# Kernel tuning notes

Measured on AMD Instinct MI355X. Metric: run time of the kernel, lower is better.

Reference implementation:

```python
import jax, jax.numpy as jnp
import numpy as np

NUM_HEAD = 16
FEAT_DIM = 1024
HEAD_DIM = FEAT_DIM // NUM_HEAD  # 64
MAX_SEQ_LEN = 2048
BATCH = 2


def setup_inputs() -> dict:
    key = jax.random.key(0)
    ks = jax.random.split(key, 6)
    x = jax.random.normal(ks[0], (BATCH, MAX_SEQ_LEN, FEAT_DIM), dtype=jnp.float32)
    # xavier_uniform: limit = sqrt(6/(fan_in+fan_out)); torch Linear weight is [out, in]
    def xavier(k, out_f, in_f):
        lim = float(np.sqrt(6.0 / (in_f + out_f)))
        return jax.random.uniform(k, (out_f, in_f), dtype=jnp.float32, minval=-lim, maxval=lim)
    W1 = xavier(ks[1], HEAD_DIM, HEAD_DIM)          # attn_mlp[0].weight
    b1 = jnp.zeros((HEAD_DIM,), dtype=jnp.float32)
    W2 = xavier(ks[2], MAX_SEQ_LEN, HEAD_DIM)       # attn_mlp[2].weight
    b2 = jnp.zeros((MAX_SEQ_LEN,), dtype=jnp.float32)
    Wv = xavier(ks[3], FEAT_DIM, FEAT_DIM)          # value_linear.weight (no bias)
    Wo = xavier(ks[4], FEAT_DIM, FEAT_DIM)          # output_linear.weight (no bias)
    return {"x": x, "W1": W1, "b1": b1, "W2": W2, "b2": b2, "Wv": Wv, "Wo": Wo}


def _split_head(t):
    b, n, _ = t.shape
    return t.reshape(b, n, NUM_HEAD, HEAD_DIM).transpose(0, 2, 1, 3)  # [b,h,n,d]


def reference(x, W1, b1, W2, b2, Wv, Wo):
    # value projection (dropout is identity in eval / p=0)
    value = x @ Wv.T                                   # [b,n,F]
    vh = _split_head(value)                            # [b,h,n,d]
    xh = _split_head(x)                                # [b,h,n,d]
    # per-head MLP -> dense attention logits [b,h,n,max_seq_len]
    hid = jax.nn.relu(jnp.einsum('bhnd,ed->bhne', xh, W1) + b1)
    logits = jnp.einsum('bhne,me->bhnm', hid, W2) + b2
    attn = jax.nn.softmax(logits, axis=-1)             # [b,h,n,m]
    out_h = jnp.einsum('bhnm,bhmd->bhnd', attn, vh)    # m == seq_len
    b_, h_, n_, d_ = out_h.shape
    out = out_h.transpose(0, 2, 1, 3).reshape(b_, n_, FEAT_DIM)
    return out @ Wo.T
```

## Files before the change

### kernel.cpp

```cpp
#include <hip/hip_runtime.h>
#include <hip/hip_bf16.h>
#include <math.h>
#include <stdint.h>


typedef __attribute__((ext_vector_type(8))) short bf16x8;
typedef __attribute__((ext_vector_type(4))) float f32x4;
typedef __attribute__((ext_vector_type(16))) float f32x16;

#define LOG2E 1.4426950408889634f

__device__ __forceinline__ unsigned short f2bf(float f) {
  union { float f; unsigned u; } v; v.f = f;
  unsigned r = v.u + 0x7FFFu + ((v.u >> 16) & 1u);
  return (unsigned short)(r >> 16);
}

__global__ __launch_bounds__(256) void conv_bf16(const float* __restrict__ src,
                                                 unsigned short* __restrict__ dst, int nq) {
  int stride = gridDim.x * blockDim.x;
  for (int q = blockIdx.x * blockDim.x + threadIdx.x; q < nq; q += stride) {
    float4 v = *(const float4*)(src + (size_t)q * 4);
    uint2 u;
    u.x = (unsigned)f2bf(v.x) | ((unsigned)f2bf(v.y) << 16);
    u.y = (unsigned)f2bf(v.z) | ((unsigned)f2bf(v.w) << 16);
    *(uint2*)(dst + (size_t)q * 4) = u;
  }
}

__global__ __launch_bounds__(256) void prep_kernel(const float* __restrict__ Wv,
                                                   const float* __restrict__ Wo,
                                                   const float* __restrict__ W2,
                                                   const float* __restrict__ W1,
                                                   const float* __restrict__ b2,
                                                   unsigned short* __restrict__ wvb,
                                                   unsigned short* __restrict__ wob,
                                                   unsigned short* __restrict__ w2b,
                                                   unsigned short* __restrict__ w1b,
                                                   float* __restrict__ eb2f,
                                                   unsigned short* __restrict__ ebb) {
  int bid = blockIdx.x;
  if (bid == 1024) {
    int i = threadIdx.x;
#pragma unroll
    for (int t = 0; t < 8; ++t) {
      int k = i * 8 + t;
      float e = __expf(b2[k]);
      eb2f[k] = e;
      ebb[k] = f2bf(e);
    }
    return;
  }
  int stride = 1024 * 256;
  for (int q = bid * 256 + threadIdx.x; q < 558080; q += stride) {
    const float* s; unsigned short* d; int o;
    if (q < 262144)      { s = Wv; d = wvb; o = q; }
    else if (q < 524288) { s = Wo; d = wob; o = q - 262144; }
    else if (q < 557056) { s = W2; d = w2b; o = q - 524288; }
    else                 { s = W1; d = w1b; o = q - 557056; }
    float4 v = *(const float4*)(s + (size_t)o * 4);
    uint2 u;
    u.x = (unsigned)f2bf(v.x) | ((unsigned)f2bf(v.y) << 16);
    u.y = (unsigned)f2bf(v.z) | ((unsigned)f2bf(v.w) << 16);
    *(uint2*)(d + (size_t)o * 4) = u;
  }
}

__device__ __forceinline__ void stage64(const char* g, size_t ldbytes, char* lds,
                                        int w, int lane) {
#pragma unroll
  for (int t = 0; t < 2; ++t) {
    int row  = w * 16 + t * 8 + (lane >> 3);
    int csrc = (lane & 7) ^ (lane >> 3);
    const char* src = g + (size_t)row * ldbytes + (csrc << 4);
    char* dst = lds + ((w * 2 + t) << 10);
    __builtin_amdgcn_global_load_lds((const __attribute__((address_space(1))) void*)src,
                                     (__attribute__((address_space(3))) void*)dst,
                                     16, 0, 0);
  }
}

__device__ __forceinline__ bf16x8 rdfrag32(const char* lds, int row, int chunk) {
  int c = chunk ^ (row & 7);
  return *(const bf16x8*)(lds + row * 128 + (c << 4));
}

__device__ __forceinline__ f32x16 loadb16(const float* p) {
  f32x16 r;
#pragma unroll
  for (int qd = 0; qd < 4; ++qd) {
    float4 v = *(const float4*)(p + qd * 8);
    r[qd * 4 + 0] = v.x; r[qd * 4 + 1] = v.y; r[qd * 4 + 2] = v.z; r[qd * 4 + 3] = v.w;
  }
  return r;
}

__device__ __forceinline__ bf16x8 pk_swap(float r0, float r1, float r2, float r3,
                                          float r4, float r5, float r6, float r7) {
  unsigned a, b, c, d;
  asm("v_cvt_pk_bf16_f32 %0, %1, %2" : "=v"(a) : "v"(r0), "v"(r1));
  asm("v_cvt_pk_bf16_f32 %0, %1, %2" : "=v"(b) : "v"(r4), "v"(r5));
  asm("v_cvt_pk_bf16_f32 %0, %1, %2" : "=v"(c) : "v"(r2), "v"(r3));
  asm("v_cvt_pk_bf16_f32 %0, %1, %2" : "=v"(d) : "v"(r6), "v"(r7));
  asm("v_permlane32_swap_b32 %0, %1" : "+v"(a), "+v"(b));
  asm("v_permlane32_swap_b32 %0, %1" : "+v"(c), "+v"(d));
  union { unsigned u[4]; bf16x8 v; } r;
  r.u[0] = a; r.u[1] = c; r.u[2] = b; r.u[3] = d;
  return r.v;
}

template<int MODE>
__global__ __launch_bounds__(256) void gemm128(const unsigned short* __restrict__ A,
                                               const unsigned short* __restrict__ B,
                                               void* __restrict__ C,
                                               const float* __restrict__ eb2f, int K) {
  __shared__ __attribute__((aligned(16))) char As[2][16384];
  __shared__ __attribute__((aligned(16))) char Bs[2][16384];
  int tid = threadIdx.x, w = tid >> 6, lane = tid & 63;
  int l31 = lane & 31, hi = lane >> 5;
  int wr = w >> 1, wc = w & 1;
  int bm = blockIdx.x, bn = blockIdx.y;
  const char* Ab = (const char*)A + (size_t)bm * 128 * (K * 2);
  const char* Bb = (const char*)B + (size_t)bn * 128 * (K * 2);
  size_t ld = (size_t)K * 2;

  f32x16 acc00 = {}, acc01 = {}, acc10 = {}, acc11 = {};
  stage64(Ab, ld, As[0], w, lane);
  stage64(Ab + 64 * ld, ld, As[0] + 8192, w, lane);
  stage64(Bb, ld, Bs[0], w, lane);
  stage64(Bb + 64 * ld, ld, Bs[0] + 8192, w, lane);
  __syncthreads();

  int nst = K >> 6;
  for (int kk = 0; kk < nst; ++kk) {
    int cur = kk & 1;
    if (kk + 1 < nst) {
      const char* An = Ab + (size_t)(kk + 1) * 128;
      const char* Bn = Bb + (size_t)(kk + 1) * 128;
      stage64(An, ld, As[cur ^ 1], w, lane);
      stage64(An + 64 * ld, ld, As[cur ^ 1] + 8192, w, lane);
      stage64(Bn, ld, Bs[cur ^ 1], w, lane);
      stage64(Bn + 64 * ld, ld, Bs[cur ^ 1] + 8192, w, lane);
    }
    __builtin_amdgcn_s_setprio(1);
#pragma unroll
    for (int ks = 0; ks < 4; ++ks) {
      bf16x8 a0 = rdfrag32(As[cur], wr * 64 + l31, ks * 2 + hi);
      bf16x8 a1 = rdfrag32(As[cur], wr * 64 + 32 + l31, ks * 2 + hi);
      bf16x8 b0 = rdfrag32(Bs[cur], wc * 64 + l31, ks * 2 + hi);
      bf16x8 b1 = rdfrag32(Bs[cur], wc * 64 + 32 + l31, ks * 2 + hi);
      acc00 = __builtin_amdgcn_mfma_f32_32x32x16_bf16(a0, b0, acc00, 0, 0, 0);
      acc01 = __builtin_amdgcn_mfma_f32_32x32x16_bf16(a0, b1, acc01, 0, 0, 0);
      acc10 = __builtin_amdgcn_mfma_f32_32x32x16_bf16(a1, b0, acc10, 0, 0, 0);
      acc11 = __builtin_amdgcn_mfma_f32_32x32x16_bf16(a1, b1, acc11, 0, 0, 0);
    }
    __builtin_amdgcn_s_setprio(0);
    __syncthreads();
  }

  if (MODE == 0) {
    unsigned short* vt = (unsigned short*)C;
#pragma unroll
    for (int i = 0; i < 2; ++i) {
      int rowb = bm * 128 + wr * 64 + i * 32;
#pragma unroll
      for (int qd = 0; qd < 4; ++qd) {
        int m0 = rowb + qd * 8 + hi * 4;
        float4 e4 = *(const float4*)(eb2f + (m0 & 2047));
        int bb = m0 >> 11, n = m0 & 2047;
#pragma unroll
        for (int j = 0; j < 2; ++j) {
          int h = bn * 2 + wc, d = j * 32 + l31;
          f32x16 a = (i == 0) ? (j == 0 ? acc00 : acc01) : (j == 0 ? acc10 : acc11);
          int r0 = qd * 4;
          uint2 u;
          u.x = (unsigned)f2bf(a[r0] * e4.x) | ((unsigned)f2bf(a[r0 + 1] * e4.y) << 16);
          u.y = (unsigned)f2bf(a[r0 + 2] * e4.z) | ((unsigned)f2bf(a[r0 + 3] * e4.w) << 16);
          *(uint2*)(vt + ((size_t)((bb * 16 + h) * 64 + d)) * 2048 + n) = u;
        }
      }
    }
  } else {
    float* Cf = (float*)C;
    int rb = bm * 128 + wr * 64, cb = bn * 128 + wc * 64;
#pragma unroll
    for (int r = 0; r < 16; ++r) {
      int row = (r & 3) + 8 * (r >> 2) + 4 * hi;
      Cf[(size_t)(rb + row) * 1024 + cb + l31]          = acc00[r];
      Cf[(size_t)(rb + row) * 1024 + cb + 32 + l31]     = acc01[r];
      Cf[(size_t)(rb + 32 + row) * 1024 + cb + l31]     = acc10[r];
      Cf[(size_t)(rb + 32 + row) * 1024 + cb + 32 + l31] = acc11[r];
    }
  }
}

__global__ __launch_bounds__(256) void flash_kernel(const unsigned short* __restrict__ xb,
                                                    const unsigned short* __restrict__ w1b,
                                                    const float* __restrict__ b1,
                                                    const unsigned short* __restrict__ w2b,
                                                    const unsigned short* __restrict__ ebb,
                                                    const unsigned short* __restrict__ vt,
                                                    unsigned short* __restrict__ aout) {
  __shared__ __attribute__((aligned(16))) char Kbuf[16384];
  __shared__ __attribute__((aligned(16))) char Vbuf[16384];
  int tid = threadIdx.x, w = tid >> 6, lane = tid & 63;
  int l31 = lane & 31, hi = lane >> 5;
  int f = blockIdx.x;
  int swz = ((f & 7) << 6) | (f >> 3);
  int qt = swz & 15, bh = swz >> 4;
  int b = bh >> 4, h = bh & 15;

  const char* px = (const char*)(xb + ((size_t)(b * 2048 + qt * 128)) * 1024 + h * 64);
  stage64(px, 2048, Kbuf, w, lane);
  stage64(px + (size_t)64 * 2048, 2048, Kbuf + 8192, w, lane);
  stage64((const char*)w1b, 128, Vbuf, w, lane);
  __syncthreads();

  f32x16 h0 = loadb16(b1 + hi * 4);
  f32x16 h1 = loadb16(b1 + 32 + hi * 4);
#pragma unroll
  for (int ks = 0; ks < 4; ++ks) {
    bf16x8 xf = rdfrag32(Kbuf, w * 32 + l31, ks * 2 + hi);
    bf16x8 wf0 = rdfrag32(Vbuf, l31, ks * 2 + hi);
    h0 = __builtin_amdgcn_mfma_f32_32x32x16_bf16(wf0, xf, h0, 0, 0, 0);
    bf16x8 wf1 = rdfrag32(Vbuf, 32 + l31, ks * 2 + hi);
    h1 = __builtin_amdgcn_mfma_f32_32x32x16_bf16(wf1, xf, h1, 0, 0, 0);
  }
#pragma unroll
  for (int i = 0; i < 16; ++i) {
    h0[i] = fmaxf(h0[i], 0.f) * LOG2E;
    h1[i] = fmaxf(h1[i], 0.f) * LOG2E;
  }
  bf16x8 qb[4];
  qb[0] = pk_swap(h0[0], h0[1], h0[2], h0[3], h0[4], h0[5], h0[6], h0[7]);
  qb[1] = pk_swap(h0[8], h0[9], h0[10], h0[11], h0[12], h0[13], h0[14], h0[15]);
  qb[2] = pk_swap(h1[0], h1[1], h1[2], h1[3], h1[4], h1[5], h1[6], h1[7]);
  qb[3] = pk_swap(h1[8], h1[9], h1[10], h1[11], h1[12], h1[13], h1[14], h1[15]);
  __syncthreads();

  const char* vtb = (const char*)vt + (size_t)bh * 64 * 4096;
  stage64((const char*)w2b, 128, Kbuf, w, lane);
  stage64(vtb, 4096, Vbuf, w, lane);

  const f32x16 zro = {};
  f32x16 oA = {}, oB = {}, L = {};
  __syncthreads();

  for (int mt = 0; mt < 32; ++mt) {
    int cur = mt & 1;
    const char* Kc = Kbuf + (cur << 13);
    const char* Vc = Vbuf + (cur << 13);
    if (mt < 31) {
      stage64((const char*)w2b + (size_t)(mt + 1) * 8192, 128, Kbuf + ((cur ^ 1) << 13), w, lane);
      stage64(vtb + (size_t)(mt + 1) * 128, 4096, Vbuf + ((cur ^ 1) << 13), w, lane);
    }
    bf16x8 ebf0 = *(const bf16x8*)(ebb + mt * 64 + hi * 8);
    bf16x8 ebf1 = *(const bf16x8*)(ebb + mt * 64 + 16 + hi * 8);
    bf16x8 ebf2 = *(const bf16x8*)(ebb + mt * 64 + 32 + hi * 8);
    bf16x8 ebf3 = *(const bf16x8*)(ebb + mt * 64 + 48 + hi * 8);

    f32x16 s0 = zro, s1 = zro;
    __builtin_amdgcn_s_setprio(1);
#pragma unroll
    for (int kt = 0; kt < 4; ++kt) {
      bf16x8 kf0 = rdfrag32(Kc, l31, kt * 2 + hi);
      s0 = __builtin_amdgcn_mfma_f32_32x32x16_bf16(kf0, qb[kt], s0, 0, 0, 0);
      bf16x8 kf1 = rdfrag32(Kc, 32 + l31, kt * 2 + hi);
      s1 = __builtin_amdgcn_mfma_f32_32x32x16_bf16(kf1, qb[kt], s1, 0, 0, 0);
    }
    __builtin_amdgcn_s_setprio(0);
#pragma unroll
    for (int i = 0; i < 16; ++i) {
      float t0, t1;
      asm("v_exp_f32 %0, %1" : "=v"(t0) : "v"(s0[i]));
      asm("v_exp_f32 %0, %1" : "=v"(t1) : "v"(s1[i]));
      s0[i] = t0; s1[i] = t1;
    }
    bf16x8 pa0 = pk_swap(s0[0], s0[1], s0[2], s0[3], s0[4], s0[5], s0[6], s0[7]);
    bf16x8 pa1 = pk_swap(s0[8], s0[9], s0[10], s0[11], s0[12], s0[13], s0[14], s0[15]);
    bf16x8 pa2 = pk_swap(s1[0], s1[1], s1[2], s1[3], s1[4], s1[5], s1[6], s1[7]);
    bf16x8 pa3 = pk_swap(s1[8], s1[9], s1[10], s1[11], s1[12], s1[13], s1[14], s1[15]);
    __builtin_amdgcn_s_setprio(1);
    L = __builtin_amdgcn_mfma_f32_32x32x16_bf16(pa0, ebf0, L, 0, 0, 0);
    L = __builtin_amdgcn_mfma_f32_32x32x16_bf16(pa1, ebf1, L, 0, 0, 0);
    L = __builtin_amdgcn_mfma_f32_32x32x16_bf16(pa2, ebf2, L, 0, 0, 0);
    L = __builtin_amdgcn_mfma_f32_32x32x16_bf16(pa3, ebf3, L, 0, 0, 0);
    {
      bf16x8 vf;
      vf = rdfrag32(Vc, l31, 0 + hi);
      oA = __builtin_amdgcn_mfma_f32_32x32x16_bf16(pa0, vf, oA, 0, 0, 0);
      vf = rdfrag32(Vc, 32 + l31, 0 + hi);
      oB = __builtin_amdgcn_mfma_f32_32x32x16_bf16(pa0, vf, oB, 0, 0, 0);
      vf = rdfrag32(Vc, l31, 2 + hi);
      oA = __builtin_amdgcn_mfma_f32_32x32x16_bf16(pa1, vf, oA, 0, 0, 0);
      vf = rdfrag32(Vc, 32 + l31, 2 + hi);
      oB = __builtin_amdgcn_mfma_f32_32x32x16_bf16(pa1, vf, oB, 0, 0, 0);
      vf = rdfrag32(Vc, l31, 4 + hi);
      oA = __builtin_amdgcn_mfma_f32_32x32x16_bf16(pa2, vf, oA, 0, 0, 0);
      vf = rdfrag32(Vc, 32 + l31, 4 + hi);
      oB = __builtin_amdgcn_mfma_f32_32x32x16_bf16(pa2, vf, oB, 0, 0, 0);
      vf = rdfrag32(Vc, l31, 6 + hi);
      oA = __builtin_amdgcn_mfma_f32_32x32x16_bf16(pa3, vf, oA, 0, 0, 0);
      vf = rdfrag32(Vc, 32 + l31, 6 + hi);
      oB = __builtin_amdgcn_mfma_f32_32x32x16_bf16(pa3, vf, oB, 0, 0, 0);
    }
    __builtin_amdgcn_s_setprio(0);
    __syncthreads();
  }

  int nb = qt * 128 + w * 32;
#pragma unroll
  for (int r = 0; r < 16; ++r) {
    float iv = 1.f / L[r];
    int ql = (r & 3) + 8 * (r >> 2) + 4 * hi;
    size_t off = ((size_t)(b * 2048 + nb + ql)) * 1024 + h * 64 + l31;
    aout[off]      = f2bf(oA[r] * iv);
    aout[off + 32] = f2bf(oB[r] * iv);
  }
}

extern "C" void kernel_launch(void* const* d_in, const int* in_sizes, int n_in,
                              void* d_out, int out_size, void* d_ws, size_t ws_size,
                              hipStream_t stream) {
  (void)in_sizes; (void)n_in; (void)out_size; (void)ws_size;
  const float* x  = (const float*)d_in[0];
  const float* W1 = (const float*)d_in[1];
  const float* b1 = (const float*)d_in[2];
  const float* W2 = (const float*)d_in[3];
  const float* b2 = (const float*)d_in[4];
  const float* Wv = (const float*)d_in[5];
  const float* Wo = (const float*)d_in[6];
  float* out = (float*)d_out;

  char* ws = (char*)d_ws;
  unsigned short* xb   = (unsigned short*)(ws);
  unsigned short* wvb  = (unsigned short*)(ws +  8388608);
  unsigned short* wob  = (unsigned short*)(ws + 10485760);
  unsigned short* w2b  = (unsigned short*)(ws + 12582912);
  unsigned short* w1b  = (unsigned short*)(ws + 12845056);
  float*          eb2f = (float*)         (ws + 12853248);
  unsigned short* ebb  = (unsigned short*)(ws + 12861440);
  unsigned short* vt   = (unsigned short*)(ws + 21233664);
  unsigned short* aout = (unsigned short*)(ws + 29622272);

  conv_bf16<<<1024, 256, 0, stream>>>(x, xb, 4194304 / 4);
  prep_kernel<<<1025, 256, 0, stream>>>(Wv, Wo, W2, W1, b2,
                                        wvb, wob, w2b, w1b, eb2f, ebb);

  gemm128<0><<<dim3(32, 8), 256, 0, stream>>>(xb, wvb, (void*)vt, eb2f, 1024);
  flash_kernel<<<512, 256, 0, stream>>>(xb, w1b, b1, w2b, ebb, vt, aout);
  gemm128<1><<<dim3(32, 8), 256, 0, stream>>>(aout, wob, (void*)out, eb2f, 1024);
}
```

Measured before the change: 101.5 us.

## Split flash kernel key range across two wave groups and merge prep kernels

The flash kernel now runs 512 threads per block. Two groups of four waves each process alternating key tiles, using a 4-deep LDS ring buffer of W2 and V tiles, and their partial outputs and row sums are combined through LDS at the end. This aims to raise wave occupancy and hide latency in the attention loop. Separately, the x conversion and weight conversion kernels are fused into one launch to remove a kernel launch. The cost is 64KB of LDS per block and an extra reduction step.

```diff
diff --git a/kernel.cpp b/kernel.cpp
--- a/kernel.cpp
+++ b/kernel.cpp
@@ -16,31 +16,21 @@
   return (unsigned short)(r >> 16);
 }
 
-__global__ __launch_bounds__(256) void conv_bf16(const float* __restrict__ src,
-                                                 unsigned short* __restrict__ dst, int nq) {
-  int stride = gridDim.x * blockDim.x;
-  for (int q = blockIdx.x * blockDim.x + threadIdx.x; q < nq; q += stride) {
-    float4 v = *(const float4*)(src + (size_t)q * 4);
-    uint2 u;
-    u.x = (unsigned)f2bf(v.x) | ((unsigned)f2bf(v.y) << 16);
-    u.y = (unsigned)f2bf(v.z) | ((unsigned)f2bf(v.w) << 16);
-    *(uint2*)(dst + (size_t)q * 4) = u;
-  }
-}
-
-__global__ __launch_bounds__(256) void prep_kernel(const float* __restrict__ Wv,
-                                                   const float* __restrict__ Wo,
-                                                   const float* __restrict__ W2,
-                                                   const float* __restrict__ W1,
-                                                   const float* __restrict__ b2,
-                                                   unsigned short* __restrict__ wvb,
-                                                   unsigned short* __restrict__ wob,
-                                                   unsigned short* __restrict__ w2b,
-                                                   unsigned short* __restrict__ w1b,
-                                                   float* __restrict__ eb2f,
-                                                   unsigned short* __restrict__ ebb) {
+__global__ __launch_bounds__(256) void prep_all(const float* __restrict__ x,
+                                                const float* __restrict__ Wv,
+                                                const float* __restrict__ Wo,
+                                                const float* __restrict__ W2,
+                                                const float* __restrict__ W1,
+                                                const float* __restrict__ b2,
+                                                unsigned short* __restrict__ xb,
+                                                unsigned short* __restrict__ wvb,
+                                                unsigned short* __restrict__ wob,
+                                                unsigned short* __restrict__ w2b,
+                                                unsigned short* __restrict__ w1b,
+                                                float* __restrict__ eb2f,
+                                                unsigned short* __restrict__ ebb) {
   int bid = blockIdx.x;
-  if (bid == 1024) {
+  if (bid == 2048) {
     int i = threadIdx.x;
 #pragma unroll
     for (int t = 0; t < 8; ++t) {
@@ -51,13 +41,17 @@
     }
     return;
   }
-  int stride = 1024 * 256;
-  for (int q = bid * 256 + threadIdx.x; q < 558080; q += stride) {
+  int stride = 2048 * 256;
+  for (int q = bid * 256 + threadIdx.x; q < 1606656; q += stride) {
     const float* s; unsigned short* d; int o;
-    if (q < 262144)      { s = Wv; d = wvb; o = q; }
-    else if (q < 524288) { s = Wo; d = wob; o = q - 262144; }
-    else if (q < 557056) { s = W2; d = w2b; o = q - 524288; }
-    else                 { s = W1; d = w1b; o = q - 557056; }
+    if (q < 1048576)      { s = x;  d = xb;  o = q; }
+    else {
+      int q2 = q - 1048576;
+      if (q2 < 262144)      { s = Wv; d = wvb; o = q2; }
+      else if (q2 < 524288) { s = Wo; d = wob; o = q2 - 262144; }
+      else if (q2 < 557056) { s = W2; d = w2b; o = q2 - 524288; }
+      else                  { s = W1; d = w1b; o = q2 - 557056; }
+    }
     float4 v = *(const float4*)(s + (size_t)o * 4);
     uint2 u;
     u.x = (unsigned)f2bf(v.x) | ((unsigned)f2bf(v.y) << 16);
@@ -78,6 +72,17 @@
                                      (__attribute__((address_space(3))) void*)dst,
                                      16, 0, 0);
   }
+}
+
+__device__ __forceinline__ void stage8(const char* g, size_t ldbytes, char* lds_,
+                                       int w, int lane) {
+  int row  = w * 8 + (lane >> 3);
+  int csrc = (lane & 7) ^ (lane >> 3);
+  const char* src = g + (size_t)row * ldbytes + (csrc << 4);
+  char* dst = lds_ + (w << 10);
+  __builtin_amdgcn_global_load_lds((const __attribute__((address_space(1))) void*)src,
+                                   (__attribute__((address_space(3))) void*)dst,
+                                   16, 0, 0);
 }
 
 __device__ __forceinline__ bf16x8 rdfrag32(const char* lds, int row, int chunk) {
@@ -194,16 +199,16 @@
   }
 }
 
-__global__ __launch_bounds__(256) void flash_kernel(const unsigned short* __restrict__ xb,
-                                                    const unsigned short* __restrict__ w1b,
-                                                    const float* __restrict__ b1,
-                                                    const unsigned short* __restrict__ w2b,
-                                                    const unsigned short* __restrict__ ebb,
-                                                    const unsigned short* __restrict__ vt,
-                                                    unsigned short* __restrict__ aout) {
-  __shared__ __attribute__((aligned(16))) char Kbuf[16384];
-  __shared__ __attribute__((aligned(16))) char Vbuf[16384];
+__global__ __launch_bounds__(512, 4) void flash_kernel(const unsigned short* __restrict__ xb,
+                                                       const unsigned short* __restrict__ w1b,
+                                                       const float* __restrict__ b1,
+                                                       const unsigned short* __restrict__ w2b,
+                                                       const unsigned short* __restrict__ ebb,
+                                                       const unsigned short* __restrict__ vt,
+                                                       unsigned short* __restrict__ aout) {
+  __shared__ __attribute__((aligned(16))) char lds[65536];
   int tid = threadIdx.x, w = tid >> 6, lane = tid & 63;
+  int wq = w & 3, grp = w >> 2;
   int l31 = lane & 31, hi = lane >> 5;
   int f = blockIdx.x;
   int swz = ((f & 7) << 6) | (f >> 3);
@@ -211,20 +216,24 @@
   int b = bh >> 4, h = bh & 15;
 
   const char* px = (const char*)(xb + ((size_t)(b * 2048 + qt * 128)) * 1024 + h * 64);
-  stage64(px, 2048, Kbuf, w, lane);
-  stage64(px + (size_t)64 * 2048, 2048, Kbuf + 8192, w, lane);
-  stage64((const char*)w1b, 128, Vbuf, w, lane);
+  stage8(px, 2048, lds, w, lane);
+  stage8(px + (size_t)64 * 2048, 2048, lds + 8192, w, lane);
+  stage8((const char*)w1b, 128, lds + 32768, w, lane);
   __syncthreads();
 
   f32x16 h0 = loadb16(b1 + hi * 4);
   f32x16 h1 = loadb16(b1 + 32 + hi * 4);
-#pragma unroll
-  for (int ks = 0; ks < 4; ++ks) {
-    bf16x8 xf = rdfrag32(Kbuf, w * 32 + l31, ks * 2 + hi);
-    bf16x8 wf0 = rdfrag32(Vbuf, l31, ks * 2 + hi);
-    h0 = __builtin_amdgcn_mfma_f32_32x32x16_bf16(wf0, xf, h0, 0, 0, 0);
-    bf16x8 wf1 = rdfrag32(Vbuf, 32 + l31, ks * 2 + hi);
-    h1 = __builtin_amdgcn_mfma_f32_32x32x16_bf16(wf1, xf, h1, 0, 0, 0);
+  {
+    const char* xt = lds + (wq >> 1) * 8192;
+    int xr = (wq & 1) * 32 + l31;
+#pragma unroll
+    for (int ks = 0; ks < 4; ++ks) {
+      bf16x8 xf = rdfrag32(xt, xr, ks * 2 + hi);
+      bf16x8 wf0 = rdfrag32(lds + 32768, l31, ks * 2 + hi);
+      h0 = __builtin_amdgcn_mfma_f32_32x32x16_bf16(wf0, xf, h0, 0, 0, 0);
+      bf16x8 wf1 = rdfrag32(lds + 32768, 32 + l31, ks * 2 + hi);
+      h1 = __builtin_amdgcn_mfma_f32_32x32x16_bf16(wf1, xf, h1, 0, 0, 0);
+    }
   }
 #pragma unroll
   for (int i = 0; i < 16; ++i) {
@@ -239,21 +248,20 @@
   __syncthreads();
 
   const char* vtb = (const char*)vt + (size_t)bh * 64 * 4096;
-  stage64((const char*)w2b, 128, Kbuf, w, lane);
-  stage64(vtb, 4096, Vbuf, w, lane);
-
+#pragma unroll
+  for (int t = 0; t < 4; ++t) {
+    stage8((const char*)w2b + (size_t)t * 8192, 128, lds + t * 8192, w, lane);
+    stage8(vtb + (size_t)t * 128, 4096, lds + 32768 + t * 8192, w, lane);
+  }
   const f32x16 zro = {};
   f32x16 oA = {}, oB = {}, L = {};
   __syncthreads();
 
-  for (int mt = 0; mt < 32; ++mt) {
-    int cur = mt & 1;
-    const char* Kc = Kbuf + (cur << 13);
-    const char* Vc = Vbuf + (cur << 13);
-    if (mt < 31) {
-      stage64((const char*)w2b + (size_t)(mt + 1) * 8192, 128, Kbuf + ((cur ^ 1) << 13), w, lane);
-      stage64(vtb + (size_t)(mt + 1) * 128, 4096, Vbuf + ((cur ^ 1) << 13), w, lane);
-    }
+  for (int s = 0; s < 16; ++s) {
+    int mt = 2 * s + grp;
+    const char* Kc = lds + (mt & 3) * 8192;
+    const char* Vc = lds + 32768 + (mt & 3) * 8192;
+
     bf16x8 ebf0 = *(const bf16x8*)(ebb + mt * 64 + hi * 8);
     bf16x8 ebf1 = *(const bf16x8*)(ebb + mt * 64 + 16 + hi * 8);
     bf16x8 ebf2 = *(const bf16x8*)(ebb + mt * 64 + 32 + hi * 8);
@@ -306,16 +314,46 @@
     }
     __builtin_amdgcn_s_setprio(0);
     __syncthreads();
-  }
-
-  int nb = qt * 128 + w * 32;
-#pragma unroll
-  for (int r = 0; r < 16; ++r) {
-    float iv = 1.f / L[r];
-    int ql = (r & 3) + 8 * (r >> 2) + 4 * hi;
-    size_t off = ((size_t)(b * 2048 + nb + ql)) * 1024 + h * 64 + l31;
-    aout[off]      = f2bf(oA[r] * iv);
-    aout[off + 32] = f2bf(oB[r] * iv);
+    if (s < 14) {
+      int t0 = 2 * s + 4, t1 = 2 * s + 5;
+      stage8((const char*)w2b + (size_t)t0 * 8192, 128, lds + (t0 & 3) * 8192, w, lane);
+      stage8(vtb + (size_t)t0 * 128, 4096, lds + 32768 + (t0 & 3) * 8192, w, lane);
+      stage8((const char*)w2b + (size_t)t1 * 8192, 128, lds + (t1 & 3) * 8192, w, lane);
+      stage8(vtb + (size_t)t1 * 128, 4096, lds + 32768 + (t1 & 3) * 8192, w, lane);
+    }
+  }
+
+  float* comb = (float*)lds;
+  if (grp == 1) {
+    float* cb = comb + (wq * 64 + lane) * 52;
+#pragma unroll
+    for (int i = 0; i < 4; ++i) {
+      *(float4*)(cb + i * 4)      = make_float4(oA[i*4], oA[i*4+1], oA[i*4+2], oA[i*4+3]);
+      *(float4*)(cb + 16 + i * 4) = make_float4(oB[i*4], oB[i*4+1], oB[i*4+2], oB[i*4+3]);
+      *(float4*)(cb + 32 + i * 4) = make_float4(L[i*4],  L[i*4+1],  L[i*4+2],  L[i*4+3]);
+    }
+  }
+  __syncthreads();
+  if (grp == 0) {
+    float* cb = comb + (wq * 64 + lane) * 52;
+#pragma unroll
+    for (int i = 0; i < 4; ++i) {
+      float4 a = *(const float4*)(cb + i * 4);
+      float4 bq = *(const float4*)(cb + 16 + i * 4);
+      float4 c = *(const float4*)(cb + 32 + i * 4);
+      oA[i*4] += a.x; oA[i*4+1] += a.y; oA[i*4+2] += a.z; oA[i*4+3] += a.w;
+      oB[i*4] += bq.x; oB[i*4+1] += bq.y; oB[i*4+2] += bq.z; oB[i*4+3] += bq.w;
+      L[i*4] += c.x;  L[i*4+1] += c.y;  L[i*4+2] += c.z;  L[i*4+3] += c.w;
+    }
+    int nb = qt * 128 + wq * 32;
+#pragma unroll
+    for (int r = 0; r < 16; ++r) {
+      float iv = 1.f / L[r];
+      int ql = (r & 3) + 8 * (r >> 2) + 4 * hi;
+      size_t off = ((size_t)(b * 2048 + nb + ql)) * 1024 + h * 64 + l31;
+      aout[off]      = f2bf(oA[r] * iv);
+      aout[off + 32] = f2bf(oB[r] * iv);
+    }
   }
 }
 
@@ -343,11 +381,10 @@
   unsigned short* vt   = (unsigned short*)(ws + 21233664);
   unsigned short* aout = (unsigned short*)(ws + 29622272);
 
-  conv_bf16<<<1024, 256, 0, stream>>>(x, xb, 4194304 / 4);
-  prep_kernel<<<1025, 256, 0, stream>>>(Wv, Wo, W2, W1, b2,
-                                        wvb, wob, w2b, w1b, eb2f, ebb);
+  prep_all<<<2049, 256, 0, stream>>>(x, Wv, Wo, W2, W1, b2,
+                                     xb, wvb, wob, w2b, w1b, eb2f, ebb);
 
   gemm128<0><<<dim3(32, 8), 256, 0, stream>>>(xb, wvb, (void*)vt, eb2f, 1024);
-  flash_kernel<<<512, 256, 0, stream>>>(xb, w1b, b1, w2b, ebb, vt, aout);
+  flash_kernel<<<512, 512, 0, stream>>>(xb, w1b, b1, w2b, ebb, vt, aout);
   gemm128<1><<<dim3(32, 8), 256, 0, stream>>>(aout, wob, (void*)out, eb2f, 1024);
 }
```

Result: faster. 98.11 us (-3.3%).
